# Performance work log

Hardware: AMD Instinct MI355X
Metric: run time of the kernel (lower is better)

## Reference

```python
import jax, jax.numpy as jnp
import numpy as np

B, S, E, H = 4, 2048, 1024, 16
D = E // H  # head_dim = 64

def setup_inputs() -> dict:
    key = jax.random.key(0)
    ks = jax.random.split(key, 9)
    std = 1.0 / np.sqrt(E)
    return {
        "x":  jax.random.normal(ks[0], (B, S, E), jnp.float32),
        "Wq": jax.random.uniform(ks[1], (E, E), jnp.float32, -std, std),
        "bq": jax.random.uniform(ks[2], (E,),   jnp.float32, -std, std),
        "Wk": jax.random.uniform(ks[3], (E, E), jnp.float32, -std, std),
        "bk": jax.random.uniform(ks[4], (E,),   jnp.float32, -std, std),
        "Wv": jax.random.uniform(ks[5], (E, E), jnp.float32, -std, std),
        "bv": jax.random.uniform(ks[6], (E,),   jnp.float32, -std, std),
        "Wo": jax.random.uniform(ks[7], (E, E), jnp.float32, -std, std),
        "bo": jax.random.uniform(ks[8], (E,),   jnp.float32, -std, std),
    }

def reference(x, Wq, bq, Wk, bk, Wv, bv, Wo, bo):
    b, s, e = x.shape
    # QKV projections (weights stored as [in,out] == torch W.T applied as x @ W)
    q = (x @ Wq + bq).reshape(b, s, H, D).transpose(0, 2, 1, 3)  # [B,H,S,D]
    k = (x @ Wk + bk).reshape(b, s, H, D).transpose(0, 2, 1, 3)
    v = (x @ Wv + bv).reshape(b, s, H, D).transpose(0, 2, 1, 3)
    scores = jnp.einsum('bhqd,bhkd->bhqk', q, k) / jnp.sqrt(jnp.float32(D))
    causal = jnp.triu(jnp.ones((s, s), bool), k=1)  # True above diagonal
    scores = jnp.where(causal, -jnp.inf, scores)
    p = jax.nn.softmax(scores, axis=-1)  # dropout disabled (eval mode)
    out = jnp.einsum('bhqk,bhkd->bhqd', p, v)  # [B,H,S,D]
    out = out.transpose(0, 2, 1, 3).reshape(b, s, e)
    return out @ Wo + bo
```

## Files before the change

kernel.cpp:

```cpp
#include <hip/hip_runtime.h>
#include <math.h>

#define E_DIM 1024
#define B_DIM 4
#define S_DIM 2048
#define H_DIM 16
#define D_HEAD 64
#define M_DIM (B_DIM * S_DIM)
#define LOG2E 1.44269504f

typedef _Float16 half8 __attribute__((ext_vector_type(8)));
typedef _Float16 half4 __attribute__((ext_vector_type(4)));
typedef __fp16  fp16x2 __attribute__((ext_vector_type(2)));
typedef float floatx4 __attribute__((ext_vector_type(4)));
#define MFMA_F16(a, b, c) __builtin_amdgcn_mfma_f32_16x16x32_f16(a, b, c, 0, 0, 0)

#if __has_builtin(__builtin_amdgcn_exp2f)
#define EXP2F(x) __builtin_amdgcn_exp2f(x)
#else
#define EXP2F(x) exp2f(x)
#endif

union H4 { fp16x2 h2[2]; half4 h4; };

#define GLDS16(g, l)                                                          \
    __builtin_amdgcn_global_load_lds(                                         \
        (const __attribute__((address_space(1))) void*)(g),                   \
        (__attribute__((address_space(3))) void*)(l), 16, 0, 0)

__device__ const int SEG_QBLK[40] = {3,4,5,6,7,7,8,8,9,9,10,10,11,11,11,12,12,12,
                                     13,13,13,14,14,14,15,15,15,15,
                                     2,6,10,14, 1,5,9,13, 0,4,8,12};
__device__ const int SEG_SEG[40]  = {0,0,0,0,0,1,0,1,0,1,0,1,0,1,2,0,1,2,
                                     0,1,2,0,1,2,0,1,2,3,
                                     0,1,2,3, 0,1,2,3, 0,1,2,3};
__device__ const int SEG_BASE[16] = {0,1,2,3,4,6,8,10,12,15,18,21,24,28,32,36};

__global__ __launch_bounds__(256) void cvt_x(
    const float* __restrict__ X, _Float16* __restrict__ Xh)
{
    size_t i = ((size_t)blockIdx.x * 256 + threadIdx.x) * 8;
    float4 a = *(const float4*)&X[i];
    float4 b = *(const float4*)&X[i + 4];
    half8 h = {(_Float16)a.x, (_Float16)a.y, (_Float16)a.z, (_Float16)a.w,
               (_Float16)b.x, (_Float16)b.y, (_Float16)b.z, (_Float16)b.w};
    *(half8*)&Xh[i] = h;
}

__global__ __launch_bounds__(256) void cvt_w(
    const float* __restrict__ W0, const float* __restrict__ W1,
    const float* __restrict__ W2, const float* __restrict__ W3,
    _Float16* __restrict__ T0, _Float16* __restrict__ T1,
    _Float16* __restrict__ T2, _Float16* __restrict__ T3)
{
    const int z = blockIdx.z;
    const float* W = (z == 0) ? W0 : (z == 1) ? W1 : (z == 2) ? W2 : W3;
    _Float16*   T  = (z == 0) ? T0 : (z == 1) ? T1 : (z == 2) ? T2 : T3;
    const int k0 = blockIdx.x * 64, n0 = blockIdx.y * 64;
    const int tid = threadIdx.x;
    __shared__ float t[64][65];
#pragma unroll
    for (int it = 0; it < 4; it++) {
        int r = it * 16 + (tid >> 4);
        int c = (tid & 15) * 4;
        float4 v = *(const float4*)&W[(size_t)(k0 + r) * E_DIM + n0 + c];
        t[r][c] = v.x; t[r][c + 1] = v.y; t[r][c + 2] = v.z; t[r][c + 3] = v.w;
    }
    __syncthreads();
#pragma unroll
    for (int it = 0; it < 2; it++) {
        int n = it * 32 + (tid >> 3);
        int kk = (tid & 7) * 8;
        half8 h;
#pragma unroll
        for (int j = 0; j < 8; j++) h[j] = (_Float16)t[kk + j][n];
        *(half8*)&T[(size_t)(n0 + n) * E_DIM + k0 + kk] = h;
    }
}

#define GEMM_CORE(Aptr, Bptr)                                                 \
    const int tid = threadIdx.x;                                              \
    const int wave = tid >> 6, lane = tid & 63;                               \
    const int m16 = lane & 15, quad = lane >> 4;                              \
    const int wm = (wave >> 1) * 64, wn = (wave & 1) * 64;                    \
    const int m0 = blockIdx.x * 128, n0 = blockIdx.y * 128;                   \
    __shared__ _Float16 As[128 * 32];                                         \
    __shared__ _Float16 Bs[128 * 32];                                         \
    floatx4 acc[4][4];                                                        \
    const floatx4 zf = {0.f, 0.f, 0.f, 0.f};                                  \
    _Pragma("unroll") for (int i = 0; i < 4; i++)                             \
        _Pragma("unroll") for (int j = 0; j < 4; j++) acc[i][j] = zf;         \
    const int lrow = lane >> 2, lseg = lane & 3;                              \
    const _Float16* gA = (Aptr) + (size_t)(m0 + wave * 32 + lrow) * E_DIM + lseg * 8; \
    const _Float16* gB = (Bptr) + (size_t)(n0 + wave * 32 + lrow) * E_DIM + lseg * 8; \
    _Float16* lA = As + (wave * 32) * 32;                                     \
    _Float16* lB = Bs + (wave * 32) * 32;                                     \
    for (int k0 = 0; k0 < E_DIM; k0 += 32) {                                  \
        __syncthreads();                                                      \
        GLDS16(gA + k0, lA);                                                  \
        GLDS16(gA + 16 * E_DIM + k0, lA + 16 * 32);                           \
        GLDS16(gB + k0, lB);                                                  \
        GLDS16(gB + 16 * E_DIM + k0, lB + 16 * 32);                           \
        __syncthreads();                                                      \
        half8 af[4], bf[4];                                                   \
        _Pragma("unroll") for (int mt = 0; mt < 4; mt++)                      \
            af[mt] = *(const half8*)&As[(wm + mt * 16 + m16) * 32 + quad * 8];\
        _Pragma("unroll") for (int nt = 0; nt < 4; nt++)                      \
            bf[nt] = *(const half8*)&Bs[(wn + nt * 16 + m16) * 32 + quad * 8];\
        _Pragma("unroll") for (int mt = 0; mt < 4; mt++)                      \
            _Pragma("unroll") for (int nt = 0; nt < 4; nt++)                  \
                acc[mt][nt] = MFMA_F16(af[mt], bf[nt], acc[mt][nt]);          \
    }

__global__ __launch_bounds__(256) void qkv_mfma(
    const _Float16* __restrict__ Xh,
    const _Float16* __restrict__ Tq, const float* __restrict__ bq,
    const _Float16* __restrict__ Tk, const float* __restrict__ bk,
    const _Float16* __restrict__ Tv, const float* __restrict__ bv,
    _Float16* __restrict__ Qo, _Float16* __restrict__ Ko, _Float16* __restrict__ Vo)
{
    const int z = blockIdx.z;
    const _Float16* Wt   = (z == 0) ? Tq : (z == 1) ? Tk : Tv;
    const float*    bias = (z == 0) ? bq : (z == 1) ? bk : bv;

    GEMM_CORE(Xh, Wt)

    if (z == 2) {
#pragma unroll
        for (int nt = 0; nt < 4; nt++) {
            int n = n0 + wn + nt * 16 + m16;
            int h = n >> 6, d = n & 63, d7 = n & 7;
            float bias_v = bias[n];
#pragma unroll
            for (int mt = 0; mt < 4; mt++) {
                int m_b = m0 + wm + mt * 16 + quad * 4;
                int b = m_b >> 11, s = m_b & 2047;
                int bh = b * H_DIM + h;
                size_t off = ((size_t)bh * 32 + (s >> 6)) * 4096
                           + (size_t)d * 64 + ((((s >> 3) & 7) ^ d7) * 8) + (s & 7);
                half4 hv;
#pragma unroll
                for (int r = 0; r < 4; r++) hv[r] = (_Float16)(acc[mt][nt][r] + bias_v);
                *(half4*)&Vo[off] = hv;
            }
        }
    } else {
        _Float16* Out = (z == 0) ? Qo : Ko;
        const float sc = (z == 0) ? 0.125f * LOG2E : 1.0f;
#pragma unroll
        for (int nt = 0; nt < 4; nt++) {
            int n = n0 + wn + nt * 16 + m16;
            int h = n >> 6;
            int db = (n >> 3) & 7, d7 = n & 7;
            float bias_v = bias[n];
#pragma unroll
            for (int mt = 0; mt < 4; mt++) {
#pragma unroll
                for (int r = 0; r < 4; r++) {
                    int m = m0 + wm + mt * 16 + quad * 4 + r;
                    int b = m >> 11, s = m & 2047;
                    int bh = b * H_DIM + h;
                    size_t off;
                    if (z == 0)
                        off = ((size_t)bh * 16 + (s >> 7)) * 8192
                            + (size_t)(s & 127) * 64 + ((db ^ (s & 7)) * 8) + d7;
                    else
                        off = ((size_t)bh * 32 + (s >> 6)) * 4096
                            + (size_t)(s & 63) * 64 + ((db ^ (s & 7)) * 8) + d7;
                    Out[off] = (_Float16)((acc[mt][nt][r] + bias_v) * sc);
                }
            }
        }
    }
}

__global__ __launch_bounds__(256) void out_mfma(
    const _Float16* __restrict__ Oh, const _Float16* __restrict__ To,
    const float* __restrict__ bias, float* __restrict__ Out)
{
    GEMM_CORE(Oh, To)

#pragma unroll
    for (int nt = 0; nt < 4; nt++) {
        int n = n0 + wn + nt * 16 + m16;
        float bias_v = bias[n];
#pragma unroll
        for (int mt = 0; mt < 4; mt++) {
#pragma unroll
            for (int r = 0; r < 4; r++) {
                int m = m0 + wm + mt * 16 + quad * 4 + r;
                Out[(size_t)m * E_DIM + n] = acc[mt][nt][r] + bias_v;
            }
        }
    }
}

__global__ __launch_bounds__(256) void attn_mfma(
    const _Float16* __restrict__ Qb, const _Float16* __restrict__ Kb,
    const _Float16* __restrict__ Vb, _Float16* __restrict__ Opart,
    float* __restrict__ Mv, float* __restrict__ Lv, _Float16* __restrict__ O)
{
    const int bh = blockIdx.y;
    const int wid = blockIdx.x;
    const int qblk = SEG_QBLK[wid];
    const int seg  = SEG_SEG[wid];
    const int q0 = qblk * 128;
    const int c0 = seg * 8;
    const int c1 = min(c0 + 8, 2 * qblk + 2);
    const bool solo = (c0 == 0) && (c1 == 2 * qblk + 2);
    const int tid = threadIdx.x;
    const int wave = tid >> 6, lane = tid & 63;
    const int m16 = lane & 15, quad = lane >> 4;
    const int sw = m16 & 7;

    __shared__ _Float16 QP[8192];
    __shared__ _Float16 KsA[8192];
    __shared__ _Float16 VsA[8192];

    const _Float16* gQ = Qb + ((size_t)bh * 16 + qblk) * 8192;
#pragma unroll
    for (int t = 0; t < 4; t++) {
        int i = wave * 4 + t;
        GLDS16(gQ + i * 512 + lane * 8, QP + i * 512);
    }

    const _Float16* kp = Kb + (size_t)bh * 131072 + (size_t)c0 * 4096 + wave * 1024 + lane * 8;
    const _Float16* vp = Vb + (size_t)bh * 131072 + (size_t)c0 * 4096 + wave * 1024 + lane * 8;
    _Float16* dK = KsA + wave * 1024;
    _Float16* dV = VsA + wave * 1024;
    {
        int b0 = (c0 & 1) * 4096;
        GLDS16(kp, dK + b0);  GLDS16(kp + 512, dK + b0 + 512);
        GLDS16(vp, dV + b0);  GLDS16(vp + 512, dV + b0 + 512);
    }
    __syncthreads();

    half8 qf[2][2];
#pragma unroll
    for (int mt = 0; mt < 2; mt++)
#pragma unroll
        for (int dh = 0; dh < 2; dh++)
            qf[mt][dh] = *(const half8*)&QP[(wave * 32 + mt * 16 + m16) * 64
                                            + (((dh * 4 + quad) ^ sw) * 8)];

    int ko[4][2], vo[4][2];
#pragma unroll
    for (int kt = 0; kt < 4; kt++) {
        ko[kt][0] = (kt * 16 + m16) * 64 + ((quad ^ sw) << 3);
        ko[kt][1] = (kt * 16 + m16) * 64 + (((quad + 4) ^ sw) << 3);
        vo[kt][0] = ko[kt][0];
        vo[kt][1] = ko[kt][1];
    }
    _Float16* Pw = QP + wave * 2048;
    _Float16* pwp[2][4];
    const _Float16* pfp[2][2];
#pragma unroll
    for (int mt = 0; mt < 2; mt++) {
#pragma unroll
        for (int kt = 0; kt < 4; kt++) {
            int kb = kt * 2 + (quad >> 1);
            pwp[mt][kt] = &Pw[(mt * 16 + m16) * 64 + ((kb ^ sw) << 3) + ((quad & 1) << 2)];
        }
#pragma unroll
        for (int kh = 0; kh < 2; kh++)
            pfp[mt][kh] = &Pw[(mt * 16 + m16) * 64 + (((kh * 4 + quad) ^ sw) << 3)];
    }

    float m_i[2] = {-INFINITY, -INFINITY}, l_i[2] = {0.f, 0.f};
    floatx4 acco[2][4];
    const floatx4 zf = {0.f, 0.f, 0.f, 0.f};
#pragma unroll
    for (int mt = 0; mt < 2; mt++)
#pragma unroll
        for (int dt = 0; dt < 4; dt++) acco[mt][dt] = zf;

    const int qmin = q0 + wave * 32;
    const int qmax = qmin + 31;

    for (int c = c0; c < c1; c++) {
        const int boff = (c & 1) * 4096;
        if (c + 1 < c1) {
            kp += 4096; vp += 4096;
            int b1 = boff ^ 4096;
            GLDS16(kp, dK + b1);  GLDS16(kp + 512, dK + b1 + 512);
            GLDS16(vp, dV + b1);  GLDS16(vp + 512, dV + b1 + 512);
        }
        const int k0 = c * 64;
        if (k0 <= qmax) {
            floatx4 sf[2][4];
#pragma unroll
            for (int kt = 0; kt < 4; kt++) {
                half8 kf0 = *(const half8*)&KsA[boff + ko[kt][0]];
                half8 kf1 = *(const half8*)&KsA[boff + ko[kt][1]];
#pragma unroll
                for (int mt = 0; mt < 2; mt++)
                    sf[mt][kt] = MFMA_F16(kf1, qf[mt][1], MFMA_F16(kf0, qf[mt][0], zf));
            }

            const bool full = (k0 + 63 <= qmin);
#pragma unroll
            for (int mt = 0; mt < 2; mt++) {
                const int qg = qmin + mt * 16 + m16;
                float p[4][4];
                float mx = -INFINITY;
#pragma unroll
                for (int kt = 0; kt < 4; kt++)
#pragma unroll
                    for (int r = 0; r < 4; r++) {
                        float v = sf[mt][kt][r];
                        if (!full) {
                            int key = k0 + kt * 16 + quad * 4 + r;
                            v = (key <= qg) ? v : -INFINITY;
                        }
                        p[kt][r] = v;
                        mx = fmaxf(mx, v);
                    }
                mx = fmaxf(mx, __shfl_xor(mx, 16));
                mx = fmaxf(mx, __shfl_xor(mx, 32));
                float mn = fmaxf(m_i[mt], mx);
                float alpha = EXP2F(m_i[mt] - mn);
                m_i[mt] = mn;
                float ls = 0.f;
#pragma unroll
                for (int kt = 0; kt < 4; kt++)
#pragma unroll
                    for (int r = 0; r < 4; r++) {
                        float e = EXP2F(p[kt][r] - mn);
                        p[kt][r] = e;
                        ls += e;
                    }
                ls += __shfl_xor(ls, 16);
                ls += __shfl_xor(ls, 32);
                l_i[mt] = l_i[mt] * alpha + ls;
#pragma unroll
                for (int dt = 0; dt < 4; dt++) acco[mt][dt] *= alpha;

#pragma unroll
                for (int kt = 0; kt < 4; kt++) {
                    H4 u;
                    u.h2[0] = __builtin_amdgcn_cvt_pkrtz(p[kt][0], p[kt][1]);
                    u.h2[1] = __builtin_amdgcn_cvt_pkrtz(p[kt][2], p[kt][3]);
                    *(half4*)pwp[mt][kt] = u.h4;
                }
            }
            asm volatile("s_waitcnt lgkmcnt(0)" ::: "memory");

            half8 pf[2][2];
#pragma unroll
            for (int mt = 0; mt < 2; mt++)
#pragma unroll
                for (int kh = 0; kh < 2; kh++)
                    pf[mt][kh] = *(const half8*)pfp[mt][kh];
#pragma unroll
            for (int dt = 0; dt < 4; dt++) {
                half8 vf0 = *(const half8*)&VsA[boff + vo[dt][0]];
                half8 vf1 = *(const half8*)&VsA[boff + vo[dt][1]];
#pragma unroll
                for (int mt = 0; mt < 2; mt++)
                    acco[mt][dt] = MFMA_F16(vf1, pf[mt][1],
                                    MFMA_F16(vf0, pf[mt][0], acco[mt][dt]));
            }
        }
        __syncthreads();
    }

    if (solo) {
        const int b = bh >> 4;
        const int h = bh & (H_DIM - 1);
#pragma unroll
        for (int mt = 0; mt < 2; mt++) {
            float inv = 1.f / l_i[mt];
            int q = qmin + mt * 16 + m16;
            _Float16* dst = O + (size_t)(b * S_DIM + q) * E_DIM + h * 64;
#pragma unroll
            for (int dt = 0; dt < 4; dt++) {
                H4 u;
                u.h2[0] = __builtin_amdgcn_cvt_pkrtz(acco[mt][dt][0] * inv, acco[mt][dt][1] * inv);
                u.h2[1] = __builtin_amdgcn_cvt_pkrtz(acco[mt][dt][2] * inv, acco[mt][dt][3] * inv);
                *(half4*)&dst[dt * 16 + quad * 4] = u.h4;
            }
        }
    } else {
        const size_t prow = ((size_t)bh * 40 + SEG_BASE[qblk] + seg) * 128;
#pragma unroll
        for (int mt = 0; mt < 2; mt++) {
            int lq = wave * 32 + mt * 16 + m16;
            if (quad == 0) {
                Mv[prow + lq] = m_i[mt];
                Lv[prow + lq] = l_i[mt];
            }
            _Float16* dst = Opart + (prow + lq) * 64;
#pragma unroll
            for (int dt = 0; dt < 4; dt++) {
                H4 u;
                u.h2[0] = __builtin_amdgcn_cvt_pkrtz(acco[mt][dt][0], acco[mt][dt][1]);
                u.h2[1] = __builtin_amdgcn_cvt_pkrtz(acco[mt][dt][2], acco[mt][dt][3]);
                *(half4*)&dst[dt * 16 + quad * 4] = u.h4;
            }
        }
    }
}

__global__ __launch_bounds__(256) void attn_combine(
    const _Float16* __restrict__ Opart, const float* __restrict__ Mv,
    const float* __restrict__ Lv, _Float16* __restrict__ O)
{
    const int qb = blockIdx.x + 4, bh = blockIdx.y;
    const int nseg = (qb >> 2) + 1;
    const size_t pbase = ((size_t)bh * 40 + SEG_BASE[qb]) * 128;
    const int t = threadIdx.x;
    const int r = t >> 1, dh = (t & 1) * 32;

    float m_s[4], w[4];
    float M = -INFINITY;
    for (int s = 0; s < nseg; s++) {
        m_s[s] = Mv[pbase + s * 128 + r];
        M = fmaxf(M, m_s[s]);
    }
    float L = 0.f;
    for (int s = 0; s < nseg; s++) {
        w[s] = EXP2F(m_s[s] - M);
        L += Lv[pbase + s * 128 + r] * w[s];
    }
    const float invL = 1.f / L;

    const int b = bh >> 4, h = bh & (H_DIM - 1);
    const int q = qb * 128 + r;
    _Float16* dst = O + (size_t)(b * S_DIM + q) * E_DIM + h * 64 + dh;
#pragma unroll
    for (int d0 = 0; d0 < 32; d0 += 8) {
        float acc[8] = {0.f, 0.f, 0.f, 0.f, 0.f, 0.f, 0.f, 0.f};
        for (int s = 0; s < nseg; s++) {
            half8 v = *(const half8*)&Opart[(pbase + s * 128 + r) * 64 + dh + d0];
#pragma unroll
            for (int j = 0; j < 8; j++) acc[j] += w[s] * (float)v[j];
        }
        half8 o;
#pragma unroll
        for (int j = 0; j < 8; j++) o[j] = (_Float16)(acc[j] * invL);
        *(half8*)&dst[d0] = o;
    }
}

extern "C" void kernel_launch(void* const* d_in, const int* in_sizes, int n_in,
                              void* d_out, int out_size, void* d_ws, size_t ws_size,
                              hipStream_t stream) {
    const float* x  = (const float*)d_in[0];
    const float* Wq = (const float*)d_in[1];
    const float* bq = (const float*)d_in[2];
    const float* Wk = (const float*)d_in[3];
    const float* bk = (const float*)d_in[4];
    const float* Wv = (const float*)d_in[5];
    const float* bv = (const float*)d_in[6];
    const float* Wo = (const float*)d_in[7];
    const float* bo = (const float*)d_in[8];

    const size_t SZ = (size_t)M_DIM * E_DIM;
    const size_t WZ = (size_t)E_DIM * E_DIM;
    _Float16* Xh = (_Float16*)d_ws;
    _Float16* Tq = Xh + SZ;
    _Float16* Tk = Tq + WZ;
    _Float16* Tv = Tk + WZ;
    _Float16* To = Tv + WZ;
    _Float16* Qb = To + WZ;
    _Float16* Kb = Qb + SZ;
    _Float16* Vb = Kb + SZ;
    _Float16* Opart = Vb + SZ;
    float* Mv = (float*)(Opart + (size_t)2560 * 8192);
    float* Lv = Mv + 2560 * 128;
    _Float16* Oh = Xh;

    cvt_x<<<dim3(M_DIM * E_DIM / 2048), 256, 0, stream>>>(x, Xh);
    cvt_w<<<dim3(16, 16, 4), 256, 0, stream>>>(Wq, Wk, Wv, Wo, Tq, Tk, Tv, To);

    qkv_mfma<<<dim3(M_DIM / 128, E_DIM / 128, 3), 256, 0, stream>>>(
        Xh, Tq, bq, Tk, bk, Tv, bv, Qb, Kb, Vb);

    attn_mfma<<<dim3(40, B_DIM * H_DIM), 256, 0, stream>>>(
        Qb, Kb, Vb, Opart, Mv, Lv, Oh);

    attn_combine<<<dim3(12, B_DIM * H_DIM), 256, 0, stream>>>(Opart, Mv, Lv, Oh);

    out_mfma<<<dim3(M_DIM / 128, E_DIM / 128), 256, 0, stream>>>(
        Oh, To, bo, (float*)d_out);
}
```

Measured before the change: 299.0 us.

## Feed P to PV MFMA from registers via 16x16x16 and shrink LDS

Instead of writing the fp16 probability tile to shared memory and reading it back in the 16x16x32 operand layout, the P fragments stay in registers and the PV product uses 16x16x16 MFMAs whose B-operand layout matches the QK output layout. V is read in half4 chunks at matching offsets. LDS is merged into one 32 KB buffer: Q is staged in the upper half and later overwritten by the double-buffered K/V tiles, with an extra barrier after the Q fragments are loaded. This removes the LDS round trip and waitcnt for P and halves LDS use, which may raise occupancy, at the cost of twice as many smaller MFMAs and more V reads.

```diff
diff --git a/kernel.cpp b/kernel.cpp
--- a/kernel.cpp
+++ b/kernel.cpp
@@ -13,7 +13,8 @@
 typedef _Float16 half4 __attribute__((ext_vector_type(4)));
 typedef __fp16  fp16x2 __attribute__((ext_vector_type(2)));
 typedef float floatx4 __attribute__((ext_vector_type(4)));
-#define MFMA_F16(a, b, c) __builtin_amdgcn_mfma_f32_16x16x32_f16(a, b, c, 0, 0, 0)
+#define MFMA_F16(a, b, c)  __builtin_amdgcn_mfma_f32_16x16x32_f16(a, b, c, 0, 0, 0)
+#define MFMA16(a, b, c)    __builtin_amdgcn_mfma_f32_16x16x16f16(a, b, c, 0, 0, 0)
 
 #if __has_builtin(__builtin_amdgcn_exp2f)
 #define EXP2F(x) __builtin_amdgcn_exp2f(x)
@@ -213,26 +214,18 @@
     const int m16 = lane & 15, quad = lane >> 4;
     const int sw = m16 & 7;
 
-    __shared__ _Float16 QP[8192];
-    __shared__ _Float16 KsA[8192];
-    __shared__ _Float16 VsA[8192];
+    __shared__ _Float16 L[16384];
 
     const _Float16* gQ = Qb + ((size_t)bh * 16 + qblk) * 8192;
 #pragma unroll
     for (int t = 0; t < 4; t++) {
         int i = wave * 4 + t;
-        GLDS16(gQ + i * 512 + lane * 8, QP + i * 512);
-    }
-
+        GLDS16(gQ + i * 512 + lane * 8, L + 8192 + i * 512);
+    }
     const _Float16* kp = Kb + (size_t)bh * 131072 + (size_t)c0 * 4096 + wave * 1024 + lane * 8;
     const _Float16* vp = Vb + (size_t)bh * 131072 + (size_t)c0 * 4096 + wave * 1024 + lane * 8;
-    _Float16* dK = KsA + wave * 1024;
-    _Float16* dV = VsA + wave * 1024;
-    {
-        int b0 = (c0 & 1) * 4096;
-        GLDS16(kp, dK + b0);  GLDS16(kp + 512, dK + b0 + 512);
-        GLDS16(vp, dV + b0);  GLDS16(vp + 512, dV + b0 + 512);
-    }
+    GLDS16(kp, L + wave * 1024);        GLDS16(kp + 512, L + wave * 1024 + 512);
+    GLDS16(vp, L + 4096 + wave * 1024); GLDS16(vp + 512, L + 4096 + wave * 1024 + 512);
     __syncthreads();
 
     half8 qf[2][2];
@@ -240,31 +233,23 @@
     for (int mt = 0; mt < 2; mt++)
 #pragma unroll
         for (int dh = 0; dh < 2; dh++)
-            qf[mt][dh] = *(const half8*)&QP[(wave * 32 + mt * 16 + m16) * 64
+            qf[mt][dh] = *(const half8*)&L[8192 + (wave * 32 + mt * 16 + m16) * 64
                                             + (((dh * 4 + quad) ^ sw) * 8)];
-
-    int ko[4][2], vo[4][2];
+    __syncthreads();
+
+    int ko[4][2];
 #pragma unroll
     for (int kt = 0; kt < 4; kt++) {
         ko[kt][0] = (kt * 16 + m16) * 64 + ((quad ^ sw) << 3);
         ko[kt][1] = (kt * 16 + m16) * 64 + (((quad + 4) ^ sw) << 3);
-        vo[kt][0] = ko[kt][0];
-        vo[kt][1] = ko[kt][1];
-    }
-    _Float16* Pw = QP + wave * 2048;
-    _Float16* pwp[2][4];
-    const _Float16* pfp[2][2];
-#pragma unroll
-    for (int mt = 0; mt < 2; mt++) {
-#pragma unroll
-        for (int kt = 0; kt < 4; kt++) {
-            int kb = kt * 2 + (quad >> 1);
-            pwp[mt][kt] = &Pw[(mt * 16 + m16) * 64 + ((kb ^ sw) << 3) + ((quad & 1) << 2)];
-        }
-#pragma unroll
-        for (int kh = 0; kh < 2; kh++)
-            pfp[mt][kh] = &Pw[(mt * 16 + m16) * 64 + (((kh * 4 + quad) ^ sw) << 3)];
-    }
+    }
+    int vx[4], vrow[4];
+#pragma unroll
+    for (int kt = 0; kt < 4; kt++)
+        vx[kt] = (((kt * 2 + (quad >> 1)) ^ sw) << 3) + ((quad & 1) << 2);
+#pragma unroll
+    for (int dt = 0; dt < 4; dt++)
+        vrow[dt] = 4096 + (dt * 16 + m16) * 64;
 
     float m_i[2] = {-INFINITY, -INFINITY}, l_i[2] = {0.f, 0.f};
     floatx4 acco[2][4];
@@ -278,26 +263,27 @@
     const int qmax = qmin + 31;
 
     for (int c = c0; c < c1; c++) {
-        const int boff = (c & 1) * 4096;
+        const int rbase = ((c - c0) & 1) * 8192;
         if (c + 1 < c1) {
             kp += 4096; vp += 4096;
-            int b1 = boff ^ 4096;
-            GLDS16(kp, dK + b1);  GLDS16(kp + 512, dK + b1 + 512);
-            GLDS16(vp, dV + b1);  GLDS16(vp + 512, dV + b1 + 512);
+            const int nb = rbase ^ 8192;
+            GLDS16(kp, L + nb + wave * 1024);        GLDS16(kp + 512, L + nb + wave * 1024 + 512);
+            GLDS16(vp, L + nb + 4096 + wave * 1024); GLDS16(vp + 512, L + nb + 4096 + wave * 1024 + 512);
         }
         const int k0 = c * 64;
         if (k0 <= qmax) {
             floatx4 sf[2][4];
 #pragma unroll
             for (int kt = 0; kt < 4; kt++) {
-                half8 kf0 = *(const half8*)&KsA[boff + ko[kt][0]];
-                half8 kf1 = *(const half8*)&KsA[boff + ko[kt][1]];
+                half8 kf0 = *(const half8*)&L[rbase + ko[kt][0]];
+                half8 kf1 = *(const half8*)&L[rbase + ko[kt][1]];
 #pragma unroll
                 for (int mt = 0; mt < 2; mt++)
                     sf[mt][kt] = MFMA_F16(kf1, qf[mt][1], MFMA_F16(kf0, qf[mt][0], zf));
             }
 
             const bool full = (k0 + 63 <= qmin);
+            half4 pk[2][4];
 #pragma unroll
             for (int mt = 0; mt < 2; mt++) {
                 const int qg = qmin + mt * 16 + m16;
@@ -334,31 +320,23 @@
                 l_i[mt] = l_i[mt] * alpha + ls;
 #pragma unroll
                 for (int dt = 0; dt < 4; dt++) acco[mt][dt] *= alpha;
-
 #pragma unroll
                 for (int kt = 0; kt < 4; kt++) {
                     H4 u;
                     u.h2[0] = __builtin_amdgcn_cvt_pkrtz(p[kt][0], p[kt][1]);
                     u.h2[1] = __builtin_amdgcn_cvt_pkrtz(p[kt][2], p[kt][3]);
-                    *(half4*)pwp[mt][kt] = u.h4;
+                    pk[mt][kt] = u.h4;
                 }
             }
-            asm volatile("s_waitcnt lgkmcnt(0)" ::: "memory");
-
-            half8 pf[2][2];
-#pragma unroll
-            for (int mt = 0; mt < 2; mt++)
-#pragma unroll
-                for (int kh = 0; kh < 2; kh++)
-                    pf[mt][kh] = *(const half8*)pfp[mt][kh];
-#pragma unroll
-            for (int dt = 0; dt < 4; dt++) {
-                half8 vf0 = *(const half8*)&VsA[boff + vo[dt][0]];
-                half8 vf1 = *(const half8*)&VsA[boff + vo[dt][1]];
-#pragma unroll
-                for (int mt = 0; mt < 2; mt++)
-                    acco[mt][dt] = MFMA_F16(vf1, pf[mt][1],
-                                    MFMA_F16(vf0, pf[mt][0], acco[mt][dt]));
+
+#pragma unroll
+            for (int kt = 0; kt < 4; kt++) {
+#pragma unroll
+                for (int dt = 0; dt < 4; dt++) {
+                    half4 vf = *(const half4*)&L[rbase + vrow[dt] + vx[kt]];
+                    acco[0][dt] = MFMA16(vf, pk[0][kt], acco[0][dt]);
+                    acco[1][dt] = MFMA16(vf, pk[1][kt], acco[1][dt]);
+                }
             }
         }
         __syncthreads();
```

Result: slower. 310.0 us (+3.7%).
